# Kernel optimization log

Hardware: AMD Instinct MI355X
Metric: run time of the kernel (lower is better)

The kernel has to match this reference:

```python
import jax, jax.numpy as jnp
import numpy as np

NUM_ENTITIES = 10000
EMB_DIM = 128   # H
FEAT_DIM = 64   # N_d
BATCH = 8192


def setup_inputs() -> dict:
    key = jax.random.key(0)
    ks = jax.random.split(key, 8)
    return {
        "e": jax.random.normal(ks[0], (NUM_ENTITIES, EMB_DIM), dtype=jnp.float32),
        "l": jax.random.normal(ks[1], (NUM_ENTITIES, FEAT_DIM), dtype=jnp.float32),
        "W_ze": jax.random.normal(ks[2], (NUM_ENTITIES, EMB_DIM, EMB_DIM), dtype=jnp.float32),
        "W_zl": jax.random.normal(ks[3], (NUM_ENTITIES, EMB_DIM, FEAT_DIM), dtype=jnp.float32),
        "W_he": jax.random.normal(ks[4], (NUM_ENTITIES, EMB_DIM, EMB_DIM), dtype=jnp.float32),
        "W_hl": jax.random.normal(ks[5], (NUM_ENTITIES, EMB_DIM, FEAT_DIM), dtype=jnp.float32),
        "b": jax.random.normal(ks[6], (EMB_DIM,), dtype=jnp.float32),
        "index": jax.random.randint(ks[7], (BATCH,), 0, NUM_ENTITIES, dtype=jnp.int64),
    }


def reference(e, l, W_ze, W_zl, W_he, W_hl, b, index):
    # Gather per-entity rows / weight matrices for the batch of ids.
    e_idx = e[index]          # [B, H]
    l_idx = l[index]          # [B, N_d]
    # Batched matvecs: 'nih,nh->ni'
    Wze = jnp.einsum('nih,nh->ni', W_ze[index], e_idx)
    Wzl = jnp.einsum('nih,nh->ni', W_zl[index], l_idx)
    Whe = jnp.einsum('nih,nh->ni', W_he[index], e_idx)
    Whl = jnp.einsum('nih,nh->ni', W_hl[index], l_idx)
    Z = jax.nn.sigmoid(Wze + Wzl + b)   # gate, [B, H]
    H = jnp.tanh(Whe + Whl)             # candidate, [B, H]
    return Z * H + (1.0 - Z) * e_idx
```

## Files before the change

### kernel.cpp

```cpp
#include <hip/hip_runtime.h>


constexpr int H_DIM = 128;
constexpr int N_D   = 64;
constexpr int N_ENT = 10000;

__global__ void k_zero_used(int* used) {
    const int i = blockIdx.x * blockDim.x + threadIdx.x;
    if (i < N_ENT) used[i] = 0;
}

__global__ void k_mark_used(const int* __restrict__ index, int* __restrict__ used, int B) {
    const int b = blockIdx.x * blockDim.x + threadIdx.x;
    if (b < B) used[index[b]] = 1;
}

__global__ __launch_bounds__(256) void k_compute_unique(
    const float* __restrict__ e,
    const float* __restrict__ l,
    const float* __restrict__ W_ze,
    const float* __restrict__ W_zl,
    const float* __restrict__ W_he,
    const float* __restrict__ W_hl,
    const float* __restrict__ bias,
    const int*  __restrict__ used,
    float* __restrict__ uout)
{
    const int bid = blockIdx.x;
    const long long n = (long long)((bid & 7) * (N_ENT / 8) + (bid >> 3));
    if (!used[n]) return;

    const int tid  = threadIdx.x;
    const int wave = tid >> 6;
    const int lane = tid & 63;
    const int g    = lane >> 4;
    const int j    = lane & 15;

    __shared__ float az_s[H_DIM];
    __shared__ float ah_s[H_DIM];

    const float4* ep = reinterpret_cast<const float4*>(e + n * H_DIM);
    const float4 xe0 = ep[j];
    const float4 xe1 = ep[j + 16];
    const float4 xl  = reinterpret_cast<const float4*>(l + n * N_D)[j];

    const float4* wze = reinterpret_cast<const float4*>(W_ze + n * (size_t)(H_DIM * H_DIM));
    const float4* whe = reinterpret_cast<const float4*>(W_he + n * (size_t)(H_DIM * H_DIM));
    const float4* wzl = reinterpret_cast<const float4*>(W_zl + n * (size_t)(H_DIM * N_D));
    const float4* whl = reinterpret_cast<const float4*>(W_hl + n * (size_t)(H_DIM * N_D));

    #pragma unroll 4
    for (int pass = 0; pass < 8; ++pass) {
        const int r = pass * 16 + wave * 4 + g;

        const float4 a0 = wze[r * 32 + j];
        const float4 a1 = wze[r * 32 + j + 16];
        const float4 b0 = whe[r * 32 + j];
        const float4 b1 = whe[r * 32 + j + 16];
        const float4 c0 = wzl[r * 16 + j];
        const float4 d0 = whl[r * 16 + j];

        float pz = fmaf(a0.x, xe0.x, fmaf(a0.y, xe0.y, fmaf(a0.z, xe0.z, a0.w * xe0.w)));
        pz = fmaf(a1.x, xe1.x, fmaf(a1.y, xe1.y, fmaf(a1.z, xe1.z, fmaf(a1.w, xe1.w, pz))));
        pz = fmaf(c0.x, xl.x,  fmaf(c0.y, xl.y,  fmaf(c0.z, xl.z,  fmaf(c0.w, xl.w,  pz))));

        float ph = fmaf(b0.x, xe0.x, fmaf(b0.y, xe0.y, fmaf(b0.z, xe0.z, b0.w * xe0.w)));
        ph = fmaf(b1.x, xe1.x, fmaf(b1.y, xe1.y, fmaf(b1.z, xe1.z, fmaf(b1.w, xe1.w, ph))));
        ph = fmaf(d0.x, xl.x,  fmaf(d0.y, xl.y,  fmaf(d0.z, xl.z,  fmaf(d0.w, xl.w,  ph))));

        #pragma unroll
        for (int m = 1; m <= 8; m <<= 1) {
            pz += __shfl_xor(pz, m, 64);
            ph += __shfl_xor(ph, m, 64);
        }
        if (j == 0) { az_s[r] = pz; ah_s[r] = ph; }
    }
    __syncthreads();

    if (tid < H_DIM) {
        const float zg = 1.0f / (1.0f + __expf(-(az_s[tid] + bias[tid])));
        const float hc = tanhf(ah_s[tid]);
        const float ei = e[n * H_DIM + tid];
        uout[n * H_DIM + tid] = zg * hc + (1.0f - zg) * ei;
    }
}

__global__ void k_gather(const int* __restrict__ index,
                         const float* __restrict__ uout,
                         float* __restrict__ out, int B)
{
    const int i = blockIdx.x * blockDim.x + threadIdx.x;
    if (i < B * (H_DIM / 4)) {
        const int b = i >> 5;
        const int c = i & 31;
        const long long n = (long long)index[b];
        reinterpret_cast<float4*>(out)[(size_t)b * 32 + c] =
            reinterpret_cast<const float4*>(uout)[n * 32 + c];
    }
}

constexpr int ELEMS = 4;
__global__ __launch_bounds__(256) void literal_e_fused(
    const float* __restrict__ e, const float* __restrict__ l,
    const float* __restrict__ W_ze, const float* __restrict__ W_zl,
    const float* __restrict__ W_he, const float* __restrict__ W_hl,
    const float* __restrict__ bias, const int* __restrict__ index,
    float* __restrict__ out)
{
    const int tid  = threadIdx.x;
    const int wave = tid >> 6;
    const int lane = tid & 63;
    const int g    = lane >> 4;
    const int j    = lane & 15;

    __shared__ float se[H_DIM];
    __shared__ float az_s[H_DIM];
    __shared__ float ah_s[H_DIM];

    const long long base = (long long)blockIdx.x * ELEMS;
    for (int it = 0; it < ELEMS; ++it) {
        const long long n  = (long long)index[base + it];
        const long long bi = base + it;
        const float4* ep = reinterpret_cast<const float4*>(e + n * H_DIM);
        const float4 xe0 = ep[j];
        const float4 xe1 = ep[j + 16];
        const float4 xl  = reinterpret_cast<const float4*>(l + n * N_D)[j];
        if (tid < H_DIM) se[tid] = e[n * H_DIM + tid];

        const float4* wze = reinterpret_cast<const float4*>(W_ze + n * (size_t)(H_DIM * H_DIM));
        const float4* whe = reinterpret_cast<const float4*>(W_he + n * (size_t)(H_DIM * H_DIM));
        const float4* wzl = reinterpret_cast<const float4*>(W_zl + n * (size_t)(H_DIM * N_D));
        const float4* whl = reinterpret_cast<const float4*>(W_hl + n * (size_t)(H_DIM * N_D));

        #pragma unroll 4
        for (int pass = 0; pass < 8; ++pass) {
            const int r = pass * 16 + wave * 4 + g;
            const float4 a0 = wze[r * 32 + j];
            const float4 a1 = wze[r * 32 + j + 16];
            const float4 b0 = whe[r * 32 + j];
            const float4 b1 = whe[r * 32 + j + 16];
            const float4 c0 = wzl[r * 16 + j];
            const float4 d0 = whl[r * 16 + j];
            float pz = fmaf(a0.x, xe0.x, fmaf(a0.y, xe0.y, fmaf(a0.z, xe0.z, a0.w * xe0.w)));
            pz = fmaf(a1.x, xe1.x, fmaf(a1.y, xe1.y, fmaf(a1.z, xe1.z, fmaf(a1.w, xe1.w, pz))));
            pz = fmaf(c0.x, xl.x,  fmaf(c0.y, xl.y,  fmaf(c0.z, xl.z,  fmaf(c0.w, xl.w,  pz))));
            float ph = fmaf(b0.x, xe0.x, fmaf(b0.y, xe0.y, fmaf(b0.z, xe0.z, b0.w * xe0.w)));
            ph = fmaf(b1.x, xe1.x, fmaf(b1.y, xe1.y, fmaf(b1.z, xe1.z, fmaf(b1.w, xe1.w, ph))));
            ph = fmaf(d0.x, xl.x,  fmaf(d0.y, xl.y,  fmaf(d0.z, xl.z,  fmaf(d0.w, xl.w,  ph))));
            #pragma unroll
            for (int m = 1; m <= 8; m <<= 1) {
                pz += __shfl_xor(pz, m, 64);
                ph += __shfl_xor(ph, m, 64);
            }
            if (j == 0) { az_s[r] = pz; ah_s[r] = ph; }
        }
        __syncthreads();
        if (tid < H_DIM) {
            const float zg = 1.0f / (1.0f + __expf(-(az_s[tid] + bias[tid])));
            const float hc = tanhf(ah_s[tid]);
            out[bi * H_DIM + tid] = zg * hc + (1.0f - zg) * se[tid];
        }
        __syncthreads();
    }
}

extern "C" void kernel_launch(void* const* d_in, const int* in_sizes, int n_in,
                              void* d_out, int out_size, void* d_ws, size_t ws_size,
                              hipStream_t stream) {
    const float* e    = (const float*)d_in[0];
    const float* l    = (const float*)d_in[1];
    const float* W_ze = (const float*)d_in[2];
    const float* W_zl = (const float*)d_in[3];
    const float* W_he = (const float*)d_in[4];
    const float* W_hl = (const float*)d_in[5];
    const float* bias = (const float*)d_in[6];
    const int*   idx  = (const int*)d_in[7];
    float* out = (float*)d_out;

    const int B = in_sizes[7];

    const size_t uout_bytes = (size_t)N_ENT * H_DIM * sizeof(float);
    const size_t need = uout_bytes + (size_t)N_ENT * sizeof(int);

    if (ws_size >= need) {
        float* uout = (float*)d_ws;
        int*   used = (int*)((char*)d_ws + uout_bytes);

        k_zero_used<<<dim3((N_ENT + 255) / 256), dim3(256), 0, stream>>>(used);
        k_mark_used<<<dim3((B + 255) / 256), dim3(256), 0, stream>>>(idx, used, B);
        k_compute_unique<<<dim3(N_ENT), dim3(256), 0, stream>>>(
            e, l, W_ze, W_zl, W_he, W_hl, bias, used, uout);
        k_gather<<<dim3((B * (H_DIM / 4) + 255) / 256), dim3(256), 0, stream>>>(
            idx, uout, out, B);
    } else {
        literal_e_fused<<<dim3(B / ELEMS), dim3(256), 0, stream>>>(
            e, l, W_ze, W_zl, W_he, W_hl, bias, idx, out);
    }
}
```

Baseline: 207.1 us.

## Compact unique entity list and split each entity's rows across four blocks

The marking kernel now uses atomics to build a compacted list of unique entity ids and a count, replacing the used-flag scan that launched a block per entity. The compute kernel launches four blocks per entity, each handling 32 output rows, and returns early for blocks beyond the unique count. The zeroing kernel becomes a hipMemsetAsync. The aim is to cut idle early-exit blocks, raise parallelism and memory-level concurrency per entity, and lose the interleaved block-to-entity mapping. In exchange the e and l vectors are reloaded four times, and the list order depends on atomic ordering, so traversal of W becomes non-sequential.

```diff
diff --git a/kernel.cpp b/kernel.cpp
--- a/kernel.cpp
+++ b/kernel.cpp
@@ -4,15 +4,18 @@
 constexpr int H_DIM = 128;
 constexpr int N_D   = 64;
 constexpr int N_ENT = 10000;
-
-__global__ void k_zero_used(int* used) {
-    const int i = blockIdx.x * blockDim.x + threadIdx.x;
-    if (i < N_ENT) used[i] = 0;
-}
-
-__global__ void k_mark_used(const int* __restrict__ index, int* __restrict__ used, int B) {
+constexpr int ROWS_PER_BLK = 32;
+
+__global__ void k_mark(const int* __restrict__ index, int* __restrict__ used,
+                       int* __restrict__ count, int* __restrict__ list, int B) {
     const int b = blockIdx.x * blockDim.x + threadIdx.x;
-    if (b < B) used[index[b]] = 1;
+    if (b < B) {
+        const int n = index[b];
+        if (atomicExch(&used[n], 1) == 0) {
+            const int p = atomicAdd(count, 1);
+            list[p] = n;
+        }
+    }
 }
 
 __global__ __launch_bounds__(256) void k_compute_unique(
@@ -23,12 +26,15 @@
     const float* __restrict__ W_he,
     const float* __restrict__ W_hl,
     const float* __restrict__ bias,
-    const int*  __restrict__ used,
+    const int*  __restrict__ count,
+    const int*  __restrict__ list,
     float* __restrict__ uout)
 {
     const int bid = blockIdx.x;
-    const long long n = (long long)((bid & 7) * (N_ENT / 8) + (bid >> 3));
-    if (!used[n]) return;
+    const int ei  = bid >> 2;
+    if (ei >= *count) return;
+    const int q = bid & 3;
+    const long long n = (long long)list[ei];
 
     const int tid  = threadIdx.x;
     const int wave = tid >> 6;
@@ -36,8 +42,8 @@
     const int g    = lane >> 4;
     const int j    = lane & 15;
 
-    __shared__ float az_s[H_DIM];
-    __shared__ float ah_s[H_DIM];
+    __shared__ float az_s[ROWS_PER_BLK];
+    __shared__ float ah_s[ROWS_PER_BLK];
 
     const float4* ep = reinterpret_cast<const float4*>(e + n * H_DIM);
     const float4 xe0 = ep[j];
@@ -49,9 +55,10 @@
     const float4* wzl = reinterpret_cast<const float4*>(W_zl + n * (size_t)(H_DIM * N_D));
     const float4* whl = reinterpret_cast<const float4*>(W_hl + n * (size_t)(H_DIM * N_D));
 
-    #pragma unroll 4
-    for (int pass = 0; pass < 8; ++pass) {
-        const int r = pass * 16 + wave * 4 + g;
+    #pragma unroll
+    for (int pass = 0; pass < 2; ++pass) {
+        const int rl = pass * 16 + wave * 4 + g;
+        const int r  = q * ROWS_PER_BLK + rl;
 
         const float4 a0 = wze[r * 32 + j];
         const float4 a1 = wze[r * 32 + j + 16];
@@ -73,15 +80,16 @@
             pz += __shfl_xor(pz, m, 64);
             ph += __shfl_xor(ph, m, 64);
         }
-        if (j == 0) { az_s[r] = pz; ah_s[r] = ph; }
+        if (j == 0) { az_s[rl] = pz; ah_s[rl] = ph; }
     }
     __syncthreads();
 
-    if (tid < H_DIM) {
-        const float zg = 1.0f / (1.0f + __expf(-(az_s[tid] + bias[tid])));
+    if (tid < ROWS_PER_BLK) {
+        const int r = q * ROWS_PER_BLK + tid;
+        const float zg = 1.0f / (1.0f + __expf(-(az_s[tid] + bias[r])));
         const float hc = tanhf(ah_s[tid]);
-        const float ei = e[n * H_DIM + tid];
-        uout[n * H_DIM + tid] = zg * hc + (1.0f - zg) * ei;
+        const float ei_v = e[n * H_DIM + r];
+        uout[n * H_DIM + r] = zg * hc + (1.0f - zg) * ei_v;
     }
 }
 
@@ -180,16 +188,18 @@
     const int B = in_sizes[7];
 
     const size_t uout_bytes = (size_t)N_ENT * H_DIM * sizeof(float);
-    const size_t need = uout_bytes + (size_t)N_ENT * sizeof(int);
+    const size_t need = uout_bytes + (size_t)(2 * N_ENT + 1) * sizeof(int);
 
     if (ws_size >= need) {
-        float* uout = (float*)d_ws;
-        int*   used = (int*)((char*)d_ws + uout_bytes);
-
-        k_zero_used<<<dim3((N_ENT + 255) / 256), dim3(256), 0, stream>>>(used);
-        k_mark_used<<<dim3((B + 255) / 256), dim3(256), 0, stream>>>(idx, used, B);
-        k_compute_unique<<<dim3(N_ENT), dim3(256), 0, stream>>>(
-            e, l, W_ze, W_zl, W_he, W_hl, bias, used, uout);
+        float* uout  = (float*)d_ws;
+        int*   used  = (int*)((char*)d_ws + uout_bytes);
+        int*   count = used + N_ENT;
+        int*   list  = count + 1;
+
+        hipMemsetAsync(used, 0, (size_t)(N_ENT + 1) * sizeof(int), stream);
+        k_mark<<<dim3((B + 255) / 256), dim3(256), 0, stream>>>(idx, used, count, list, B);
+        k_compute_unique<<<dim3(4 * N_ENT), dim3(256), 0, stream>>>(
+            e, l, W_ze, W_zl, W_he, W_hl, bias, count, list, uout);
         k_gather<<<dim3((B * (H_DIM / 4) + 255) / 256), dim3(256), 0, stream>>>(
             idx, uout, out, B);
     } else {
```

Result: no change. 209.4 us (+1.1%).
